# Optimization experiments

Hardware: AMD Instinct MI355X
Metric: run time of the kernel (lower is better)

The kernel has to match this reference:

```python
import jax, jax.numpy as jnp
import numpy as np


def setup_inputs() -> dict:
    key = jax.random.key(0)
    B, N, H, S = 16, 512, 8, 64
    # batch: sorted graph ids, each graph has exactly N nodes
    batch = (jnp.arange(B * N) // N).astype(jnp.int32)
    # all intra-graph node pairs (Graphormer SPD is all-pairs per graph)
    offs = (jnp.arange(B, dtype=jnp.int32) * N)[:, None, None]  # [B,1,1]
    base = jnp.arange(N, dtype=jnp.int32)
    src = jnp.broadcast_to(offs + base[None, :, None], (B, N, N)).reshape(-1)
    dst = jnp.broadcast_to(offs + base[None, None, :], (B, N, N)).reshape(-1)
    graph_index = jnp.stack([src, dst])  # [2, E], E = B*N*N
    k1, k2, k3 = jax.random.split(key, 3)
    spatial_types = jax.random.randint(k1, (B * N * N,), 0, S + 1, dtype=jnp.int32)
    emb_weight = 0.02 * jax.random.normal(k2, (S + 1, H), dtype=jnp.float32)
    graph_token = 0.02 * jax.random.normal(k3, (1, H, 1), dtype=jnp.float32)
    return {"spatial_types": spatial_types, "graph_index": graph_index,
            "batch": batch, "num_graphs": B, "max_nodes": N,
            "emb_weight": emb_weight, "graph_token": graph_token}


def reference(spatial_types, graph_index, batch, num_graphs, max_nodes, emb_weight, graph_token):
    B, N = num_graphs, max_nodes
    H = emb_weight.shape[1]
    num_nodes = batch.shape[0]
    # local (within-graph) node index, as in to_dense_adj
    counts = jax.ops.segment_sum(jnp.ones_like(batch), batch, num_segments=B)
    ptr = jnp.concatenate([jnp.zeros((1,), counts.dtype), jnp.cumsum(counts)[:-1]])
    local = jnp.arange(num_nodes, dtype=batch.dtype) - ptr[batch]
    g = batch[graph_index[0]]
    i = local[graph_index[0]]
    j = local[graph_index[1]]
    emb = emb_weight[spatial_types]  # [E, H] embedding gather
    # scatter-add into dense adjacency [B, N, N, H]
    adj = jnp.zeros((B, N, N, H), dtype=emb.dtype).at[g, i, j].add(emb)
    bias = adj.transpose(0, 3, 1, 2)  # [B, H, N, N]
    # pad one row/col at the front for the graph token
    bias = jnp.pad(bias, ((0, 0), (0, 0), (1, 0), (1, 0)))
    bias = bias.at[:, :, 1:, 0].set(jnp.broadcast_to(graph_token, (B, H, N)))
    bias = bias.at[:, :, 0, :].set(jnp.broadcast_to(graph_token, (B, H, N + 1)))
    return bias.reshape(B * H, N + 1, N + 1)
```

## Files before the change

kernel.cpp:

```cpp
#include <hip/hip_runtime.h>

#define BGR   16
#define NNODE 512
#define NH    8
#define NP1   513
#define PLANE (NP1 * NP1)
#define NTYPE 65

typedef float f32x4 __attribute__((ext_vector_type(4)));

__device__ __forceinline__ int P(int j) { return j + (j >> 5); }

__global__ __launch_bounds__(256) void bias_rowblk_kernel(
    const int*   __restrict__ st,
    const float* __restrict__ emb,
    const float* __restrict__ token,
    float*       __restrict__ out)
{
    __shared__ float lemb[NH * NTYPE];
    __shared__ float ltok[NH];
    __shared__ int   sstp[528];

    const int tid = threadIdx.x;
    const int b   = blockIdx.y;
    const int rid = blockIdx.x;

    for (int t = tid; t < NH * NTYPE; t += 256)
        lemb[(t & 7) * NTYPE + (t >> 3)] = emb[t];
    if (tid < NH) ltok[tid] = token[tid];

    if (rid == NNODE) {
        __syncthreads();
        for (int t = tid; t < NH * NP1; t += 256) {
            int h = t / NP1;
            int c = t - h * NP1;
            out[(unsigned)(b * NH + h) * PLANE + c] = ltok[h];
        }
        return;
    }

    if (tid < 128) {
        const int4* srow4 = reinterpret_cast<const int4*>(st)
                          + (b * NNODE + rid) * (NNODE / 4);
        int4 w = srow4[tid];
        int pj = 4 * tid + (tid >> 3);
        sstp[pj]     = w.x;
        sstp[pj + 1] = w.y;
        sstp[pj + 2] = w.z;
        sstp[pj + 3] = w.w;
    }
    __syncthreads();

    const int r    = rid + 1;
    const int wave = tid >> 6;
    const int lane = tid & 63;

    #pragma unroll
    for (int hh = 0; hh < 2; ++hh) {
        const int h = wave * 2 + hh;
        const unsigned gh = (unsigned)(b * NH + h) * (unsigned)PLANE
                          + (unsigned)r * NP1;
        const int a = (int)((0u - gh) & 3u);
        const int K = (NP1 - a) >> 2;
        const float* __restrict__ le = lemb + h * NTYPE;
        const float tok = ltok[h];

        #pragma unroll
        for (int jj = 0; jj < 2; ++jj) {
            const int i = lane + 64 * jj;
            if (jj == 1 && i >= K) continue;
            const int col = a + 4 * i;
            const int ib  = col - 1;
            f32x4 val;
            #pragma unroll
            for (int k = 0; k < 4; ++k) {
                int idx = ib + k;
                if (idx < 0) idx = 0;
                val[k] = le[sstp[P(idx)]];
            }
            if (col == 0) val[0] = tok;
            *reinterpret_cast<f32x4*>(out + gh + col) = val;
        }

        const int ns = NP1 - 4 * K;
        if (lane < ns) {
            const int col = (lane < a) ? lane : 4 * K + lane;
            float v = (col == 0) ? tok : le[sstp[P(col - 1)]];
            out[gh + col] = v;
        }
    }
}

extern "C" void kernel_launch(void* const* d_in, const int* in_sizes, int n_in,
                              void* d_out, int out_size, void* d_ws, size_t ws_size,
                              hipStream_t stream) {
    const int*   spatial_types = (const int*)  d_in[0];
    const float* emb_weight    = (const float*)d_in[5];
    const float* graph_token   = (const float*)d_in[6];
    float*       out           = (float*)d_out;

    dim3 grid(NP1, BGR);
    bias_rowblk_kernel<<<grid, dim3(256), 0, stream>>>(
        spatial_types, emb_weight, graph_token, out);
}
```

Baseline: 178.6 us.

## Process eight rows per block with double-buffered LDS staging of spatial types

Each block now handles eight consecutive rows instead of one. It loads all eight rows of spatial types into registers up front and stages them through a double-buffered shared array while the output rows are written. This amortizes the per-block embedding-table load and launch overhead across more rows and exposes several global loads at once. In exchange the grid shrinks from about 8k to about 1k blocks, the kernel uses more registers, and one sync is added per row.

```diff
diff --git a/kernel.cpp b/kernel.cpp
--- a/kernel.cpp
+++ b/kernel.cpp
@@ -6,12 +6,14 @@
 #define NP1   513
 #define PLANE (NP1 * NP1)
 #define NTYPE 65
+#define RPB   8
+#define NGRP  (NNODE / RPB)
 
 typedef float f32x4 __attribute__((ext_vector_type(4)));
 
 __device__ __forceinline__ int P(int j) { return j + (j >> 5); }
 
-__global__ __launch_bounds__(256) void bias_rowblk_kernel(
+__global__ __launch_bounds__(256) void bias_pipe_kernel(
     const int*   __restrict__ st,
     const float* __restrict__ emb,
     const float* __restrict__ token,
@@ -19,17 +21,17 @@
 {
     __shared__ float lemb[NH * NTYPE];
     __shared__ float ltok[NH];
-    __shared__ int   sstp[528];
+    __shared__ int   sstp[2][528];
 
     const int tid = threadIdx.x;
     const int b   = blockIdx.y;
-    const int rid = blockIdx.x;
+    const int grp = blockIdx.x;
 
     for (int t = tid; t < NH * NTYPE; t += 256)
         lemb[(t & 7) * NTYPE + (t >> 3)] = emb[t];
     if (tid < NH) ltok[tid] = token[tid];
 
-    if (rid == NNODE) {
+    if (grp == NGRP) {
         __syncthreads();
         for (int t = tid; t < NH * NP1; t += 256) {
             int h = t / NP1;
@@ -39,54 +41,75 @@
         return;
     }
 
+    const int row0 = grp * RPB;
+    int4 w[RPB];
     if (tid < 128) {
-        const int4* srow4 = reinterpret_cast<const int4*>(st)
-                          + (b * NNODE + rid) * (NNODE / 4);
-        int4 w = srow4[tid];
-        int pj = 4 * tid + (tid >> 3);
-        sstp[pj]     = w.x;
-        sstp[pj + 1] = w.y;
-        sstp[pj + 2] = w.z;
-        sstp[pj + 3] = w.w;
+        const int4* stb = reinterpret_cast<const int4*>(st)
+                        + (size_t)(b * NNODE + row0) * (NNODE / 4);
+        #pragma unroll
+        for (int q = 0; q < RPB; ++q)
+            w[q] = stb[q * (NNODE / 4) + tid];
+        const int pj = 4 * tid + (tid >> 3);
+        sstp[0][pj]     = w[0].x;
+        sstp[0][pj + 1] = w[0].y;
+        sstp[0][pj + 2] = w[0].z;
+        sstp[0][pj + 3] = w[0].w;
     }
     __syncthreads();
 
-    const int r    = rid + 1;
     const int wave = tid >> 6;
     const int lane = tid & 63;
 
     #pragma unroll
-    for (int hh = 0; hh < 2; ++hh) {
-        const int h = wave * 2 + hh;
-        const unsigned gh = (unsigned)(b * NH + h) * (unsigned)PLANE
-                          + (unsigned)r * NP1;
-        const int a = (int)((0u - gh) & 3u);
-        const int K = (NP1 - a) >> 2;
-        const float* __restrict__ le = lemb + h * NTYPE;
-        const float tok = ltok[h];
+    for (int q = 0; q < RPB; ++q) {
+        const int cur = q & 1;
+        const int r   = row0 + q + 1;
+        const int* __restrict__ sp = sstp[cur];
 
         #pragma unroll
-        for (int jj = 0; jj < 2; ++jj) {
-            const int i = lane + 64 * jj;
-            if (jj == 1 && i >= K) continue;
-            const int col = a + 4 * i;
-            const int ib  = col - 1;
-            f32x4 val;
+        for (int hh = 0; hh < 2; ++hh) {
+            const int h = wave * 2 + hh;
+            const unsigned gh = (unsigned)(b * NH + h) * (unsigned)PLANE
+                              + (unsigned)r * NP1;
+            const int a = (int)((0u - gh) & 3u);
+            const int K = (NP1 - a) >> 2;
+            const float* __restrict__ le = lemb + h * NTYPE;
+            const float tok = ltok[h];
+
             #pragma unroll
-            for (int k = 0; k < 4; ++k) {
-                int idx = ib + k;
-                if (idx < 0) idx = 0;
-                val[k] = le[sstp[P(idx)]];
+            for (int jj = 0; jj < 2; ++jj) {
+                const int i = lane + 64 * jj;
+                if (jj == 1 && i >= K) continue;
+                const int col = a + 4 * i;
+                const int ib  = col - 1;
+                f32x4 val;
+                #pragma unroll
+                for (int k = 0; k < 4; ++k) {
+                    int idx = ib + k;
+                    if (idx < 0) idx = 0;
+                    val[k] = le[sp[P(idx)]];
+                }
+                if (col == 0) val[0] = tok;
+                *reinterpret_cast<f32x4*>(out + gh + col) = val;
             }
-            if (col == 0) val[0] = tok;
-            *reinterpret_cast<f32x4*>(out + gh + col) = val;
+
+            const int ns = NP1 - 4 * K;
+            if (lane < ns) {
+                const int col = (lane < a) ? lane : 4 * K + lane;
+                out[gh + col] = (col == 0) ? tok : le[sp[P(col - 1)]];
+            }
         }
 
-        const int ns = NP1 - 4 * K;
-        if (lane < ns) {
-            const int col = (lane < a) ? lane : 4 * K + lane;
-            float v = (col == 0) ? tok : le[sstp[P(col - 1)]];
-            out[gh + col] = v;
+        if (q + 1 < RPB) {
+            if (tid < 128) {
+                const int nb = (q + 1) & 1;
+                const int pj = 4 * tid + (tid >> 3);
+                sstp[nb][pj]     = w[q + 1].x;
+                sstp[nb][pj + 1] = w[q + 1].y;
+                sstp[nb][pj + 2] = w[q + 1].z;
+                sstp[nb][pj + 3] = w[q + 1].w;
+            }
+            __syncthreads();
         }
     }
 }
@@ -99,7 +122,7 @@
     const float* graph_token   = (const float*)d_in[6];
     float*       out           = (float*)d_out;
 
-    dim3 grid(NP1, BGR);
-    bias_rowblk_kernel<<<grid, dim3(256), 0, stream>>>(
+    dim3 grid(NGRP + 1, BGR);
+    bias_pipe_kernel<<<grid, dim3(256), 0, stream>>>(
         spatial_types, emb_weight, graph_token, out);
 }
```

Result: no change. 176.9 us (-1.0%).

## Assign one output row per wave covering all heads to cut blocks and barriers

Applied to the files above, without the earlier changes.

Work is redistributed so each wave owns one graph row and writes all eight head planes for it. Before, each block handled one row and its four waves split the heads. Each wave loads its own row of spatial types into a private LDS slice with no block barrier after the load, and the grid shrinks from 513 to 129 blocks per graph. The aim is to remove the per-row barrier and block-launch overhead and to give each wave more independent stores in flight. Skipping the barrier relies on lanes of the same wave seeing each other's LDS writes without explicit synchronisation. Each wave also does four times more serial work, which lowers the number of waves available to hide latency.

```diff
diff --git a/kernel.cpp b/kernel.cpp
--- a/kernel.cpp
+++ b/kernel.cpp
@@ -11,7 +11,7 @@
 
 __device__ __forceinline__ int P(int j) { return j + (j >> 5); }
 
-__global__ __launch_bounds__(256) void bias_rowblk_kernel(
+__global__ __launch_bounds__(256) void bias_wave_kernel(
     const int*   __restrict__ st,
     const float* __restrict__ emb,
     const float* __restrict__ token,
@@ -19,45 +19,47 @@
 {
     __shared__ float lemb[NH * NTYPE];
     __shared__ float ltok[NH];
-    __shared__ int   sstp[528];
+    __shared__ int   sstp[4][528];
 
     const int tid = threadIdx.x;
     const int b   = blockIdx.y;
-    const int rid = blockIdx.x;
 
     for (int t = tid; t < NH * NTYPE; t += 256)
         lemb[(t & 7) * NTYPE + (t >> 3)] = emb[t];
     if (tid < NH) ltok[tid] = token[tid];
+    __syncthreads();
 
-    if (rid == NNODE) {
-        __syncthreads();
+    if (blockIdx.x == 128) {
         for (int t = tid; t < NH * NP1; t += 256) {
-            int h = t / NP1;
-            int c = t - h * NP1;
+            const int h = t / NP1;
+            const int c = t - h * NP1;
             out[(unsigned)(b * NH + h) * PLANE + c] = ltok[h];
         }
         return;
     }
 
-    if (tid < 128) {
-        const int4* srow4 = reinterpret_cast<const int4*>(st)
-                          + (b * NNODE + rid) * (NNODE / 4);
-        int4 w = srow4[tid];
-        int pj = 4 * tid + (tid >> 3);
-        sstp[pj]     = w.x;
-        sstp[pj + 1] = w.y;
-        sstp[pj + 2] = w.z;
-        sstp[pj + 3] = w.w;
-    }
-    __syncthreads();
-
-    const int r    = rid + 1;
     const int wave = tid >> 6;
     const int lane = tid & 63;
+    const int r    = blockIdx.x * 4 + wave + 1;
+
+    const int4* __restrict__ srow4 = reinterpret_cast<const int4*>(st)
+                                   + (size_t)(b * NNODE + (r - 1)) * (NNODE / 4);
+    const int4 w0 = srow4[lane];
+    const int4 w1 = srow4[lane + 64];
+
+    int* __restrict__ sp = sstp[wave];
+    {
+        const int p0 = 4 * lane + (lane >> 3);
+        sp[p0]     = w0.x; sp[p0 + 1] = w0.y;
+        sp[p0 + 2] = w0.z; sp[p0 + 3] = w0.w;
+        const int j1 = 256 + 4 * lane;
+        const int p1 = j1 + 8 + (lane >> 3);
+        sp[p1]     = w1.x; sp[p1 + 1] = w1.y;
+        sp[p1 + 2] = w1.z; sp[p1 + 3] = w1.w;
+    }
 
     #pragma unroll
-    for (int hh = 0; hh < 2; ++hh) {
-        const int h = wave * 2 + hh;
+    for (int h = 0; h < NH; ++h) {
         const unsigned gh = (unsigned)(b * NH + h) * (unsigned)PLANE
                           + (unsigned)r * NP1;
         const int a = (int)((0u - gh) & 3u);
@@ -76,7 +78,7 @@
             for (int k = 0; k < 4; ++k) {
                 int idx = ib + k;
                 if (idx < 0) idx = 0;
-                val[k] = le[sstp[P(idx)]];
+                val[k] = le[sp[P(idx)]];
             }
             if (col == 0) val[0] = tok;
             *reinterpret_cast<f32x4*>(out + gh + col) = val;
@@ -85,8 +87,7 @@
         const int ns = NP1 - 4 * K;
         if (lane < ns) {
             const int col = (lane < a) ? lane : 4 * K + lane;
-            float v = (col == 0) ? tok : le[sstp[P(col - 1)]];
-            out[gh + col] = v;
+            out[gh + col] = (col == 0) ? tok : le[sp[P(col - 1)]];
         }
     }
 }
@@ -99,7 +100,7 @@
     const float* graph_token   = (const float*)d_in[6];
     float*       out           = (float*)d_out;
 
-    dim3 grid(NP1, BGR);
-    bias_rowblk_kernel<<<grid, dim3(256), 0, stream>>>(
+    dim3 grid(129, BGR);
+    bias_wave_kernel<<<grid, dim3(256), 0, stream>>>(
         spatial_types, emb_weight, graph_token, out);
 }
```

New measurement: 177.6 us. About the same (-0.6%).
